# Kernel optimization log

Hardware: AMD Instinct MI355X
Metric: run time of the kernel (lower is better)

Reference implementation:

```python
import jax, jax.numpy as jnp
import numpy as np

H = 64
VOCAB = 128
LN_EPS = 1e-5
NORM_EPS = 1e-12


def _l2norm(k):
    # F.normalize(..., dim=-1): x / max(||x||_2, eps)
    n = jnp.sqrt(jnp.sum(k * k, axis=-1, keepdims=True))
    return k / jnp.maximum(n, NORM_EPS)


def _delta_scan(M0, ks, vs):
    # ks, vs: [L, B, H] time-major; M0: [B, H, H]
    def step(M, kv):
        k, v = kv
        Mk = jnp.einsum('bij,bj->bi', M, k)            # [B,H]
        M = M + (v - Mk)[:, :, None] * k[:, None, :]   # rank-1 update
        return M, None
    M, _ = jax.lax.scan(step, M0, (ks, vs))
    return M


def reference(x, embed, W1, b1, W2, b2, ln_g, ln_b, Wk, Wv, Wq, Wattn, Wout, bout):
    # Encoder: embed -> residual FF -> LayerNorm
    h = embed[x]                                        # [B,L,H]
    ff = jnp.maximum(h @ W1.T + b1, 0.0) @ W2.T + b2
    z = h + ff
    mu = jnp.mean(z, axis=-1, keepdims=True)
    var = jnp.mean((z - mu) ** 2, axis=-1, keepdims=True)
    hidden = (z - mu) / jnp.sqrt(var + LN_EPS) * ln_g + ln_b  # [B,L,H]

    B, L, _ = hidden.shape
    # First delta-rule memory write over all L steps
    ks = _l2norm(hidden @ Wk.T)                         # [B,L,H]
    vs = hidden @ Wv.T                                  # [B,L,H]
    M0 = jnp.zeros((B, H, H), dtype=hidden.dtype)
    M = _delta_scan(M0, jnp.swapaxes(ks, 0, 1), jnp.swapaxes(vs, 0, 1))

    half = L // 2
    slots = jnp.swapaxes(M, 1, 2)                       # [B,H,H] = M^T
    q = hidden[:, :half, :] @ Wattn.T                   # [B,half,H]
    # bmm(q, slots^T) = q @ M
    attn = jax.nn.softmax(jnp.einsum('bth,bhk->btk', q, M) / jnp.sqrt(jnp.asarray(H, hidden.dtype)), axis=-1)
    ctx = jnp.einsum('btk,bkh->bth', attn, slots)       # [B,half,H]

    # Second delta-rule write seeded from M
    ks2 = _l2norm(ctx @ Wk.T)
    vs2 = ctx @ Wv.T
    M2 = _delta_scan(M, jnp.swapaxes(ks2, 0, 1), jnp.swapaxes(vs2, 0, 1))

    q_last = hidden[:, -1, :] @ Wq.T                    # [B,H]
    read = jnp.einsum('bij,bj->bi', M2, q_last)         # [B,H]
    return read @ Wout.T + bout                         # [B,VOCAB]


def setup_inputs() -> dict:
    key = jax.random.key(0)
    ks = jax.random.split(key, 16)
    B, L = 64, 4096
    s = 0.05
    return {
        'x': jax.random.randint(ks[0], (B, L), 0, VOCAB),
        'embed': jax.random.normal(ks[1], (VOCAB, H), jnp.float32) * s,
        'W1': jax.random.normal(ks[2], (2 * H, H), jnp.float32) * s,
        'b1': jnp.zeros((2 * H,), jnp.float32),
        'W2': jax.random.normal(ks[3], (H, 2 * H), jnp.float32) * s,
        'b2': jnp.zeros((H,), jnp.float32),
        'ln_g': jnp.ones((H,), jnp.float32),
        'ln_b': jnp.zeros((H,), jnp.float32),
        'Wk': jax.random.normal(ks[4], (H, H), jnp.float32) * s,
        'Wv': jax.random.normal(ks[5], (H, H), jnp.float32) * s,
        'Wq': jax.random.normal(ks[6], (H, H), jnp.float32) * s,
        'Wattn': jax.random.normal(ks[7], (H, H), jnp.float32) * s,
        'Wout': jax.random.normal(ks[8], (VOCAB, H), jnp.float32) * s,
        'bout': jnp.zeros((VOCAB,), jnp.float32),
    }
```

## Files before the change

kernel.cpp:

```cpp
#include <hip/hip_runtime.h>

#define SEQL 4096
#define NB 64

__device__ __forceinline__ float dpp_xor1_add(float x) {
    int v = __builtin_amdgcn_mov_dpp(__float_as_int(x), 0xB1, 0xF, 0xF, true);
    return x + __int_as_float(v);
}
__device__ __forceinline__ float dpp_xor2_add(float x) {
    int v = __builtin_amdgcn_mov_dpp(__float_as_int(x), 0x4E, 0xF, 0xF, true);
    return x + __int_as_float(v);
}

#define FMA16(A, W, H)                                      \
    A[0]  = fmaf(W.x, H.x, A[0]);  A[1]  = fmaf(W.x, H.y, A[1]);   \
    A[2]  = fmaf(W.x, H.z, A[2]);  A[3]  = fmaf(W.x, H.w, A[3]);   \
    A[4]  = fmaf(W.y, H.x, A[4]);  A[5]  = fmaf(W.y, H.y, A[5]);   \
    A[6]  = fmaf(W.y, H.z, A[6]);  A[7]  = fmaf(W.y, H.w, A[7]);   \
    A[8]  = fmaf(W.z, H.x, A[8]);  A[9]  = fmaf(W.z, H.y, A[9]);   \
    A[10] = fmaf(W.z, H.z, A[10]); A[11] = fmaf(W.z, H.w, A[11]);  \
    A[12] = fmaf(W.w, H.x, A[12]); A[13] = fmaf(W.w, H.y, A[13]);  \
    A[14] = fmaf(W.w, H.z, A[14]); A[15] = fmaf(W.w, H.w, A[15])

__device__ __forceinline__ void proj_tile64(const float* __restrict__ sW,
                                            const float* __restrict__ sA,
                                            int jq, int tq, float* __restrict__ a)
{
#pragma unroll
    for (int u = 0; u < 16; ++u) a[u] = 0.f;
#pragma unroll 2
    for (int i = 0; i < 64; ++i) {
        float4 w  = *reinterpret_cast<const float4*>(&sW[i * 68 + jq]);
        float4 h4 = *reinterpret_cast<const float4*>(&sA[i * 68 + tq]);
        FMA16(a, w, h4);
    }
}

__device__ __forceinline__ void stage_w_t(const float* __restrict__ W, int ldw, int col0,
                                          float* __restrict__ sWb, int tid)
{
#pragma unroll
    for (int it = 0; it < 4; ++it) {
        int item = it * 256 + tid;
        int j = item & 63, cq = item >> 6;
        float4 w = *reinterpret_cast<const float4*>(&W[(size_t)j * ldw + col0 + cq * 4]);
        sWb[(cq * 4 + 0) * 68 + j] = w.x;
        sWb[(cq * 4 + 1) * 68 + j] = w.y;
        sWb[(cq * 4 + 2) * 68 + j] = w.z;
        sWb[(cq * 4 + 3) * 68 + j] = w.w;
    }
}

__device__ __forceinline__ void stage_w_n(const float* __restrict__ W,
                                          float* __restrict__ sWb, int tid)
{
#pragma unroll
    for (int it = 0; it < 4; ++it) {
        int item = it * 256 + tid;
        int r = item >> 4, c4 = item & 15;
        float4 w = *reinterpret_cast<const float4*>(&W[(size_t)r * 64 + c4 * 4]);
        *reinterpret_cast<float4*>(&sWb[r * 68 + c4 * 4]) = w;
    }
}

__global__ __launch_bounds__(256) void encoder_kernel(
    const int* __restrict__ x, const float* __restrict__ embed,
    const float* __restrict__ W1, const float* __restrict__ b1,
    const float* __restrict__ W2, const float* __restrict__ b2,
    const float* __restrict__ ln_g, const float* __restrict__ ln_b,
    const float* __restrict__ Wk, const float* __restrict__ Wv,
    const float* __restrict__ Wq, const float* __restrict__ Wattn,
    float* __restrict__ ks, float* __restrict__ vs,
    float* __restrict__ qbuf, float* __restrict__ qlast)
{
    __shared__ __align__(16) float sZ[64 * 68];
    __shared__ __align__(16) float sF[64 * 68];
    __shared__ __align__(16) float sW[64 * 68];

    const int tid = threadIdx.x;
    const size_t g0 = (size_t)blockIdx.x * 64;
    const int b = (int)(g0 >> 12);
    const int l0 = (int)(g0 & (SEQL - 1));
    const int jq = (tid & 15) * 4;
    const int tq = (tid >> 4) * 4;

    for (int idx = tid; idx < 4096; idx += 256) {
        int t = idx >> 6, i = idx & 63;
        sZ[i * 68 + t] = embed[(size_t)x[g0 + t] * 64 + i];
    }

    float zacc[16];
#pragma unroll
    for (int u = 0; u < 16; ++u) zacc[u] = 0.f;
    for (int ph = 0; ph < 2; ++ph) {
        if (ph) __syncthreads();
        stage_w_t(W1 + (size_t)ph * 64 * 64, 64, 0, sW, tid);
        __syncthreads();
        float a[16];
        proj_tile64(sW, sZ, jq, tq, a);
        float4 bb = *reinterpret_cast<const float4*>(&b1[ph * 64 + jq]);
        float bv[4] = {bb.x, bb.y, bb.z, bb.w};
#pragma unroll
        for (int u = 0; u < 4; ++u) {
            float4 o;
            o.x = fmaxf(a[u * 4 + 0] + bv[u], 0.f);
            o.y = fmaxf(a[u * 4 + 1] + bv[u], 0.f);
            o.z = fmaxf(a[u * 4 + 2] + bv[u], 0.f);
            o.w = fmaxf(a[u * 4 + 3] + bv[u], 0.f);
            *reinterpret_cast<float4*>(&sF[(jq + u) * 68 + tq]) = o;
        }
        __syncthreads();
        stage_w_t(W2, 128, ph * 64, sW, tid);
        __syncthreads();
#pragma unroll 2
        for (int p = 0; p < 64; ++p) {
            float4 w  = *reinterpret_cast<const float4*>(&sW[p * 68 + jq]);
            float4 f4 = *reinterpret_cast<const float4*>(&sF[p * 68 + tq]);
            FMA16(zacc, w, f4);
        }
    }

    {
        float z[16];
        float4 b2v = *reinterpret_cast<const float4*>(&b2[jq]);
        float bv[4] = {b2v.x, b2v.y, b2v.z, b2v.w};
#pragma unroll
        for (int u = 0; u < 4; ++u) {
            float4 h4 = *reinterpret_cast<const float4*>(&sZ[(jq + u) * 68 + tq]);
            z[u * 4 + 0] = h4.x + bv[u] + zacc[u * 4 + 0];
            z[u * 4 + 1] = h4.y + bv[u] + zacc[u * 4 + 1];
            z[u * 4 + 2] = h4.z + bv[u] + zacc[u * 4 + 2];
            z[u * 4 + 3] = h4.w + bv[u] + zacc[u * 4 + 3];
        }
        float s[4], ss[4];
#pragma unroll
        for (int v = 0; v < 4; ++v) {
            s[v]  = z[v] + z[4 + v] + z[8 + v] + z[12 + v];
            ss[v] = z[v] * z[v] + z[4 + v] * z[4 + v]
                  + z[8 + v] * z[8 + v] + z[12 + v] * z[12 + v];
        }
#pragma unroll
        for (int m = 1; m <= 8; m <<= 1) {
#pragma unroll
            for (int v = 0; v < 4; ++v) {
                s[v]  += __shfl_xor(s[v], m);
                ss[v] += __shfl_xor(ss[v], m);
            }
        }
        float mu[4], inv[4];
#pragma unroll
        for (int v = 0; v < 4; ++v) {
            mu[v] = s[v] * 0.015625f;
            float var = ss[v] * 0.015625f - mu[v] * mu[v];
            inv[v] = rsqrtf(var + 1e-5f);
        }
        float4 g4  = *reinterpret_cast<const float4*>(&ln_g[jq]);
        float4 be4 = *reinterpret_cast<const float4*>(&ln_b[jq]);
        float gv[4] = {g4.x, g4.y, g4.z, g4.w};
        float bev[4] = {be4.x, be4.y, be4.z, be4.w};
#pragma unroll
        for (int u = 0; u < 4; ++u) {
            float4 o;
            o.x = (z[u * 4 + 0] - mu[0]) * inv[0] * gv[u] + bev[u];
            o.y = (z[u * 4 + 1] - mu[1]) * inv[1] * gv[u] + bev[u];
            o.z = (z[u * 4 + 2] - mu[2]) * inv[2] * gv[u] + bev[u];
            o.w = (z[u * 4 + 3] - mu[3]) * inv[3] * gv[u] + bev[u];
            *reinterpret_cast<float4*>(&sZ[(jq + u) * 68 + tq]) = o;
        }
    }

    {
        __syncthreads();
        stage_w_t(Wk, 64, 0, sW, tid);
        __syncthreads();
        float a[16];
        proj_tile64(sW, sZ, jq, tq, a);
        float ssq[4];
#pragma unroll
        for (int v = 0; v < 4; ++v)
            ssq[v] = a[v] * a[v] + a[4 + v] * a[4 + v]
                   + a[8 + v] * a[8 + v] + a[12 + v] * a[12 + v];
#pragma unroll
        for (int m = 1; m <= 8; m <<= 1) {
#pragma unroll
            for (int v = 0; v < 4; ++v) ssq[v] += __shfl_xor(ssq[v], m);
        }
#pragma unroll
        for (int v = 0; v < 4; ++v) {
            float sc = 1.f / fmaxf(sqrtf(ssq[v]), 1e-12f);
            float4 o = make_float4(a[v] * sc, a[4 + v] * sc, a[8 + v] * sc, a[12 + v] * sc);
            *reinterpret_cast<float4*>(&ks[(g0 + tq + v) * 64 + jq]) = o;
        }
    }

    {
        __syncthreads();
        stage_w_t(Wv, 64, 0, sW, tid);
        __syncthreads();
        float a[16];
        proj_tile64(sW, sZ, jq, tq, a);
#pragma unroll
        for (int v = 0; v < 4; ++v) {
            float4 o = make_float4(a[v], a[4 + v], a[8 + v], a[12 + v]);
            *reinterpret_cast<float4*>(&vs[(g0 + tq + v) * 64 + jq]) = o;
        }
    }

    if (l0 < 2048) {
        __syncthreads();
        stage_w_t(Wattn, 64, 0, sW, tid);
        __syncthreads();
        float a[16];
        proj_tile64(sW, sZ, jq, tq, a);
#pragma unroll
        for (int v = 0; v < 4; ++v) {
            float4 o = make_float4(a[v], a[4 + v], a[8 + v], a[12 + v]);
            *reinterpret_cast<float4*>(&qbuf[((size_t)b * 2048 + l0 + tq + v) * 64 + jq]) = o;
        }
    }

    if (l0 == SEQL - 64) {
        __syncthreads();
        stage_w_t(Wq, 64, 0, sW, tid);
        __syncthreads();
        float a[16];
        proj_tile64(sW, sZ, jq, tq, a);
        if ((tid >> 4) == 15) {
            float4 o = make_float4(a[3], a[7], a[11], a[15]);
            *reinterpret_cast<float4*>(&qlast[(size_t)b * 64 + jq]) = o;
        }
    }
}

#define STEP2(K0, K1, K2, K3, V)                                                \
    do {                                                                        \
        float dp0 = fmaf(p[0], K0.x, fmaf(p[1], K0.y, fmaf(p[2], K0.z, p[3] * K0.w))); \
        float dp1 = fmaf(p[4], K1.x, fmaf(p[5], K1.y, fmaf(p[6], K1.z, p[7] * K1.w))); \
        float dp2 = fmaf(p[8], K2.x, fmaf(p[9], K2.y, fmaf(p[10], K2.z, p[11] * K2.w))); \
        float dp3 = fmaf(p[12], K3.x, fmaf(p[13], K3.y, fmaf(p[14], K3.z, p[15] * K3.w))); \
        float dq0 = fmaf(q[0], K0.x, fmaf(q[1], K0.y, fmaf(q[2], K0.z, q[3] * K0.w))); \
        float dq1 = fmaf(q[4], K1.x, fmaf(q[5], K1.y, fmaf(q[6], K1.z, q[7] * K1.w))); \
        float dq2 = fmaf(q[8], K2.x, fmaf(q[9], K2.y, fmaf(q[10], K2.z, q[11] * K2.w))); \
        float dq3 = fmaf(q[12], K3.x, fmaf(q[13], K3.y, fmaf(q[14], K3.z, q[15] * K3.w))); \
        float ddp = (dp0 + dp1) + (dp2 + dp3);                                  \
        float ddq = (dq0 + dq1) + (dq2 + dq3);                                  \
        ddp = dpp_xor1_add(ddp);  ddq = dpp_xor1_add(ddq);                      \
        ddp = dpp_xor2_add(ddp);  ddq = dpp_xor2_add(ddq);                      \
        float up = -ddp;                                                        \
        float uq = V - ddq;                                                     \
        p[0] = fmaf(up, K0.x, p[0]);   q[0] = fmaf(uq, K0.x, q[0]);             \
        p[1] = fmaf(up, K0.y, p[1]);   q[1] = fmaf(uq, K0.y, q[1]);             \
        p[2] = fmaf(up, K0.z, p[2]);   q[2] = fmaf(uq, K0.z, q[2]);             \
        p[3] = fmaf(up, K0.w, p[3]);   q[3] = fmaf(uq, K0.w, q[3]);             \
        p[4] = fmaf(up, K1.x, p[4]);   q[4] = fmaf(uq, K1.x, q[4]);             \
        p[5] = fmaf(up, K1.y, p[5]);   q[5] = fmaf(uq, K1.y, q[5]);             \
        p[6] = fmaf(up, K1.z, p[6]);   q[6] = fmaf(uq, K1.z, q[6]);             \
        p[7] = fmaf(up, K1.w, p[7]);   q[7] = fmaf(uq, K1.w, q[7]);             \
        p[8] = fmaf(up, K2.x, p[8]);   q[8] = fmaf(uq, K2.x, q[8]);             \
        p[9] = fmaf(up, K2.y, p[9]);   q[9] = fmaf(uq, K2.y, q[9]);             \
        p[10] = fmaf(up, K2.z, p[10]); q[10] = fmaf(uq, K2.z, q[10]);           \
        p[11] = fmaf(up, K2.w, p[11]); q[11] = fmaf(uq, K2.w, q[11]);           \
        p[12] = fmaf(up, K3.x, p[12]); q[12] = fmaf(uq, K3.x, q[12]);           \
        p[13] = fmaf(up, K3.y, p[13]); q[13] = fmaf(uq, K3.y, q[13]);           \
        p[14] = fmaf(up, K3.z, p[14]); q[14] = fmaf(uq, K3.z, q[14]);           \
        p[15] = fmaf(up, K3.w, p[15]); q[15] = fmaf(uq, K3.w, q[15]);           \
    } while (0)

__global__ __launch_bounds__(256) void chunk_kernel(
    float* __restrict__ ksb, float* __restrict__ vsb, int C)
{
    __shared__ __align__(16) float sk[2][32 * 64];
    __shared__ __align__(16) float sv[2][32 * 64];

    const int job = blockIdx.x;
    const int tid = threadIdx.x;
    const int r = tid >> 2;
    const int c0 = (tid & 3) * 16;
    float* kc = ksb + (size_t)job * C * 64;
    float* vc = vsb + (size_t)job * C * 64;

    float p[16], q[16];
#pragma unroll
    for (int j = 0; j < 16; ++j) { p[j] = (c0 + j == r) ? 1.f : 0.f; q[j] = 0.f; }

    const int nt = C >> 5;
    float4 rk0, rk1, rv0, rv1;

    {
        const float4* gk = reinterpret_cast<const float4*>(kc);
        const float4* gv = reinterpret_cast<const float4*>(vc);
        float4 a0 = gk[tid], a1 = gk[256 + tid];
        float4 b0 = gv[tid], b1 = gv[256 + tid];
        float4* dk = reinterpret_cast<float4*>(sk[0]);
        float4* dv = reinterpret_cast<float4*>(sv[0]);
        dk[tid] = a0; dk[256 + tid] = a1;
        dv[tid] = b0; dv[256 + tid] = b1;
    }
    if (nt > 1) {
        const float4* gk = reinterpret_cast<const float4*>(kc + 2048);
        const float4* gv = reinterpret_cast<const float4*>(vc + 2048);
        rk0 = gk[tid]; rk1 = gk[256 + tid];
        rv0 = gv[tid]; rv1 = gv[256 + tid];
    }
    __syncthreads();

    int cur = 0;
    for (int tile = 0; tile < nt; ++tile) {
        if (tile + 1 < nt) {
            float4* dk = reinterpret_cast<float4*>(sk[cur ^ 1]);
            float4* dv = reinterpret_cast<float4*>(sv[cur ^ 1]);
            dk[tid] = rk0; dk[256 + tid] = rk1;
            dv[tid] = rv0; dv[256 + tid] = rv1;
            if (tile + 2 < nt) {
                const float4* gk = reinterpret_cast<const float4*>(kc + (size_t)(tile + 2) * 2048);
                const float4* gv = reinterpret_cast<const float4*>(vc + (size_t)(tile + 2) * 2048);
                rk0 = gk[tid]; rk1 = gk[256 + tid];
                rv0 = gv[tid]; rv1 = gv[256 + tid];
            }
        }

        const float* kl = sk[cur] + c0;
        const float* vl = sv[cur] + r;
        float4 a0, a1, a2, a3, e0, e1, e2, e3;
        float va, ve;
        {
            const float4* kp = reinterpret_cast<const float4*>(kl);
            a0 = kp[0]; a1 = kp[1]; a2 = kp[2]; a3 = kp[3];
            va = vl[0];
        }
#pragma unroll
        for (int t = 0; t < 32; t += 2) {
            {
                const float4* kp = reinterpret_cast<const float4*>(kl + (t + 1) * 64);
                e0 = kp[0]; e1 = kp[1]; e2 = kp[2]; e3 = kp[3];
                ve = vl[(t + 1) * 64];
            }
            STEP2(a0, a1, a2, a3, va);
            if (t + 2 < 32) {
                const float4* kp = reinterpret_cast<const float4*>(kl + (t + 2) * 64);
                a0 = kp[0]; a1 = kp[1]; a2 = kp[2]; a3 = kp[3];
                va = vl[(t + 2) * 64];
            }
            STEP2(e0, e1, e2, e3, ve);
        }
        __syncthreads();
        cur ^= 1;
    }

    float4* po = reinterpret_cast<float4*>(kc + r * 64 + c0);
    po[0] = make_float4(p[0], p[1], p[2], p[3]);
    po[1] = make_float4(p[4], p[5], p[6], p[7]);
    po[2] = make_float4(p[8], p[9], p[10], p[11]);
    po[3] = make_float4(p[12], p[13], p[14], p[15]);
    float4* qo = reinterpret_cast<float4*>(vc + r * 64 + c0);
    qo[0] = make_float4(q[0], q[1], q[2], q[3]);
    qo[1] = make_float4(q[4], q[5], q[6], q[7]);
    qo[2] = make_float4(q[8], q[9], q[10], q[11]);
    qo[3] = make_float4(q[12], q[13], q[14], q[15]);
}

__global__ __launch_bounds__(256) void combine_kernel(
    const float* __restrict__ Pb, const float* __restrict__ Qb,
    const float* __restrict__ Min, float* __restrict__ Mout,
    int nc, int chunk_stride)
{
    __shared__ __align__(16) float sM[2][64 * 68];
    __shared__ __align__(16) float sP[2][64 * 64];
    const int b = blockIdx.x;
    const int tid = threadIdx.x;
    const int r = tid >> 2;
    const int j0 = (tid & 3) * 16;

    if (Min) {
        const float4* mi = reinterpret_cast<const float4*>(Min + ((size_t)b * 64 + r) * 64 + j0);
        float4* mo = reinterpret_cast<float4*>(&sM[0][r * 68 + j0]);
#pragma unroll
        for (int u = 0; u < 4; ++u) mo[u] = mi[u];
    } else {
#pragma unroll
        for (int u = 0; u < 16; ++u) sM[0][r * 68 + j0 + u] = 0.f;
    }
    {
        const float4* g = reinterpret_cast<const float4*>(Pb + (size_t)b * nc * chunk_stride);
        float4* s = reinterpret_cast<float4*>(sP[0]);
        for (int i = tid; i < 1024; i += 256) s[i] = g[i];
    }
    __syncthreads();

    int cur = 0;
    for (int c = 0; c < nc; ++c) {
        const size_t cbase = (size_t)(b * nc + c) * chunk_stride;
        float4 rp0, rp1, rp2, rp3;
        if (c + 1 < nc) {
            const float4* g = reinterpret_cast<const float4*>(Pb + cbase + chunk_stride);
            rp0 = g[tid]; rp1 = g[tid + 256]; rp2 = g[tid + 512]; rp3 = g[tid + 768];
        }
        float4 rq0, rq1, rq2, rq3;
        {
            const float4* gq = reinterpret_cast<const float4*>(Qb + cbase + r * 64 + j0);
            rq0 = gq[0]; rq1 = gq[1]; rq2 = gq[2]; rq3 = gq[3];
        }
        float acc[16];
#pragma unroll
        for (int u = 0; u < 16; ++u) acc[u] = 0.f;
        const float* Mrow = &sM[cur][r * 68];
        const float* Pl = sP[c & 1];
#pragma unroll
        for (int mg = 0; mg < 16; ++mg) {
            float4 a = *reinterpret_cast<const float4*>(Mrow + mg * 4);
#pragma unroll
            for (int e2 = 0; e2 < 4; ++e2) {
                float am = (e2 == 0) ? a.x : (e2 == 1) ? a.y : (e2 == 2) ? a.z : a.w;
                const float4* pr = reinterpret_cast<const float4*>(Pl + (mg * 4 + e2) * 64 + j0);
                float4 p0 = pr[0], p1 = pr[1], p2 = pr[2], p3 = pr[3];
                acc[0] = fmaf(am, p0.x, acc[0]);  acc[1] = fmaf(am, p0.y, acc[1]);
                acc[2] = fmaf(am, p0.z, acc[2]);  acc[3] = fmaf(am, p0.w, acc[3]);
                acc[4] = fmaf(am, p1.x, acc[4]);  acc[5] = fmaf(am, p1.y, acc[5]);
                acc[6] = fmaf(am, p1.z, acc[6]);  acc[7] = fmaf(am, p1.w, acc[7]);
                acc[8] = fmaf(am, p2.x, acc[8]);  acc[9] = fmaf(am, p2.y, acc[9]);
                acc[10] = fmaf(am, p2.z, acc[10]); acc[11] = fmaf(am, p2.w, acc[11]);
                acc[12] = fmaf(am, p3.x, acc[12]); acc[13] = fmaf(am, p3.y, acc[13]);
                acc[14] = fmaf(am, p3.z, acc[14]); acc[15] = fmaf(am, p3.w, acc[15]);
            }
        }
        const int nxt = cur ^ 1;
        float* om = &sM[nxt][r * 68 + j0];
        om[0] = acc[0] + rq0.x;  om[1] = acc[1] + rq0.y;
        om[2] = acc[2] + rq0.z;  om[3] = acc[3] + rq0.w;
        om[4] = acc[4] + rq1.x;  om[5] = acc[5] + rq1.y;
        om[6] = acc[6] + rq1.z;  om[7] = acc[7] + rq1.w;
        om[8] = acc[8] + rq2.x;  om[9] = acc[9] + rq2.y;
        om[10] = acc[10] + rq2.z; om[11] = acc[11] + rq2.w;
        om[12] = acc[12] + rq3.x; om[13] = acc[13] + rq3.y;
        om[14] = acc[14] + rq3.z; om[15] = acc[15] + rq3.w;
        if (c + 1 < nc) {
            float4* s = reinterpret_cast<float4*>(sP[(c + 1) & 1]);
            s[tid] = rp0; s[tid + 256] = rp1; s[tid + 512] = rp2; s[tid + 768] = rp3;
        }
        __syncthreads();
        cur = nxt;
    }

    float4* mo = reinterpret_cast<float4*>(Mout + ((size_t)b * 64 + r) * 64 + j0);
    const float* fm = &sM[cur][r * 68 + j0];
    mo[0] = make_float4(fm[0], fm[1], fm[2], fm[3]);
    mo[1] = make_float4(fm[4], fm[5], fm[6], fm[7]);
    mo[2] = make_float4(fm[8], fm[9], fm[10], fm[11]);
    mo[3] = make_float4(fm[12], fm[13], fm[14], fm[15]);
}

__global__ __launch_bounds__(256) void attn_kernel(
    const float* __restrict__ qg, const float* __restrict__ Mbuf,
    const float* __restrict__ Wk, const float* __restrict__ Wv,
    float* __restrict__ ks2, float* __restrict__ vs2)
{
    __shared__ __align__(16) float sW1[64 * 68];
    __shared__ __align__(16) float sW2[64 * 68];
    __shared__ __align__(16) float sA[64 * 68];
    __shared__ __align__(16) float sB[64 * 68];

    const int b = blockIdx.y;
    const int tile0 = blockIdx.x * 64;
    const int tid = threadIdx.x;
    const int jq = (tid & 15) * 4;
    const int tq = (tid >> 4) * 4;
    const size_t qbase = (size_t)b * 2048 + tile0;
    const float* Mb = Mbuf + (size_t)b * 4096;

    stage_w_n(Mb, sW1, tid);
    stage_w_t(Mb, 64, 0, sW2, tid);
    stage_w_t(qg + qbase * 64, 64, 0, sA, tid);
    __syncthreads();

    float a[16];
    proj_tile64(sW1, sA, jq, tq, a);
#pragma unroll
    for (int u = 0; u < 16; ++u) a[u] *= 0.125f;

    {
        float mx[4], sm[4];
#pragma unroll
        for (int v = 0; v < 4; ++v)
            mx[v] = fmaxf(fmaxf(a[v], a[4 + v]), fmaxf(a[8 + v], a[12 + v]));
#pragma unroll
        for (int m = 1; m <= 8; m <<= 1) {
#pragma unroll
            for (int v = 0; v < 4; ++v) mx[v] = fmaxf(mx[v], __shfl_xor(mx[v], m));
        }
#pragma unroll
        for (int v = 0; v < 4; ++v) {
            a[v]      = __expf(a[v]      - mx[v]);
            a[4 + v]  = __expf(a[4 + v]  - mx[v]);
            a[8 + v]  = __expf(a[8 + v]  - mx[v]);
            a[12 + v] = __expf(a[12 + v] - mx[v]);
            sm[v] = a[v] + a[4 + v] + a[8 + v] + a[12 + v];
        }
#pragma unroll
        for (int m = 1; m <= 8; m <<= 1) {
#pragma unroll
            for (int v = 0; v < 4; ++v) sm[v] += __shfl_xor(sm[v], m);
        }
        float rinv[4];
#pragma unroll
        for (int v = 0; v < 4; ++v) rinv[v] = 1.f / sm[v];
#pragma unroll
        for (int v = 0; v < 4; ++v) {
            a[v] *= rinv[v]; a[4 + v] *= rinv[v];
            a[8 + v] *= rinv[v]; a[12 + v] *= rinv[v];
        }
    }
#pragma unroll
    for (int u = 0; u < 4; ++u)
        *reinterpret_cast<float4*>(&sB[(jq + u) * 68 + tq]) =
            make_float4(a[u * 4 + 0], a[u * 4 + 1], a[u * 4 + 2], a[u * 4 + 3]);
    __syncthreads();

    float c[16];
    proj_tile64(sW2, sB, jq, tq, c);
#pragma unroll
    for (int u = 0; u < 4; ++u)
        *reinterpret_cast<float4*>(&sA[(jq + u) * 68 + tq]) =
            make_float4(c[u * 4 + 0], c[u * 4 + 1], c[u * 4 + 2], c[u * 4 + 3]);
    __syncthreads();

    stage_w_t(Wk, 64, 0, sW1, tid);
    stage_w_t(Wv, 64, 0, sW2, tid);
    __syncthreads();

    float ak[16], av[16];
#pragma unroll
    for (int u = 0; u < 16; ++u) { ak[u] = 0.f; av[u] = 0.f; }
#pragma unroll 2
    for (int i = 0; i < 64; ++i) {
        float4 wk = *reinterpret_cast<const float4*>(&sW1[i * 68 + jq]);
        float4 wv = *reinterpret_cast<const float4*>(&sW2[i * 68 + jq]);
        float4 c4 = *reinterpret_cast<const float4*>(&sA[i * 68 + tq]);
        FMA16(ak, wk, c4);
        FMA16(av, wv, c4);
    }

    {
        float ssq[4];
#pragma unroll
        for (int v = 0; v < 4; ++v)
            ssq[v] = ak[v] * ak[v] + ak[4 + v] * ak[4 + v]
                   + ak[8 + v] * ak[8 + v] + ak[12 + v] * ak[12 + v];
#pragma unroll
        for (int m = 1; m <= 8; m <<= 1) {
#pragma unroll
            for (int v = 0; v < 4; ++v) ssq[v] += __shfl_xor(ssq[v], m);
        }
#pragma unroll
        for (int v = 0; v < 4; ++v) {
            float sc = 1.f / fmaxf(sqrtf(ssq[v]), 1e-12f);
            const size_t o = (qbase + tq + v) * 64 + jq;
            *reinterpret_cast<float4*>(&ks2[o]) =
                make_float4(ak[v] * sc, ak[4 + v] * sc, ak[8 + v] * sc, ak[12 + v] * sc);
            *reinterpret_cast<float4*>(&vs2[o]) =
                make_float4(av[v], av[4 + v], av[8 + v], av[12 + v]);
        }
    }
}

__global__ __launch_bounds__(128) void out_kernel(
    const float* __restrict__ M2, const float* __restrict__ qlast,
    const float* __restrict__ Wout, const float* __restrict__ bout,
    float* __restrict__ out)
{
    const int b = blockIdx.x;
    const int tid = threadIdx.x;
    __shared__ float sq[64], sread[64];
    if (tid < 64) sq[tid] = qlast[b * 64 + tid];
    __syncthreads();
    if (tid < 64) {
        const float* Mr = M2 + ((size_t)b * 64 + tid) * 64;
        float acc = 0.f;
        for (int j = 0; j < 64; ++j) acc = fmaf(Mr[j], sq[j], acc);
        sread[tid] = acc;
    }
    __syncthreads();
    float acc = bout[tid];
    for (int h = 0; h < 64; ++h) acc = fmaf(Wout[tid * 64 + h], sread[h], acc);
    out[b * 128 + tid] = acc;
}

extern "C" void kernel_launch(void* const* d_in, const int* in_sizes, int n_in,
                              void* d_out, int out_size, void* d_ws, size_t ws_size,
                              hipStream_t stream)
{
    const int* x        = (const int*)d_in[0];
    const float* embed  = (const float*)d_in[1];
    const float* W1     = (const float*)d_in[2];
    const float* b1     = (const float*)d_in[3];
    const float* W2     = (const float*)d_in[4];
    const float* b2     = (const float*)d_in[5];
    const float* ln_g   = (const float*)d_in[6];
    const float* ln_b   = (const float*)d_in[7];
    const float* Wk     = (const float*)d_in[8];
    const float* Wv     = (const float*)d_in[9];
    const float* Wq     = (const float*)d_in[10];
    const float* Wattn  = (const float*)d_in[11];
    const float* Wout   = (const float*)d_in[12];
    const float* bout   = (const float*)d_in[13];

    float* ws = (float*)d_ws;
    float* ks = ws;
    float* vs = ks + (size_t)NB * SEQL * 64;
    float* qb = vs + (size_t)NB * SEQL * 64;
    float* ql = qb + (size_t)NB * 2048 * 64;
    float* M  = ql + (size_t)NB * 64;
    float* M2 = M + (size_t)NB * 64 * 64;
    if (ws_size < (size_t)(M2 + (size_t)NB * 64 * 64 - ws) * sizeof(float)) return;

    hipLaunchKernelGGL(encoder_kernel, dim3((NB * SEQL) / 64), dim3(256), 0, stream,
                       x, embed, W1, b1, W2, b2, ln_g, ln_b, Wk, Wv, Wq, Wattn,
                       ks, vs, qb, ql);

    const int C1 = 256, nc1 = SEQL / C1;
    hipLaunchKernelGGL(chunk_kernel, dim3(NB * nc1), dim3(256), 0, stream, ks, vs, C1);
    hipLaunchKernelGGL(combine_kernel, dim3(NB), dim3(256), 0, stream,
                       ks, vs, (const float*)nullptr, M, nc1, C1 * 64);

    hipLaunchKernelGGL(attn_kernel, dim3(32, NB), dim3(256), 0, stream,
                       qb, M, Wk, Wv, ks, vs);

    const int C2 = 128, nc2 = 2048 / C2;
    hipLaunchKernelGGL(chunk_kernel, dim3(NB * nc2), dim3(256), 0, stream, ks, vs, C2);
    hipLaunchKernelGGL(combine_kernel, dim3(NB), dim3(256), 0, stream,
                       ks, vs, M, M2, nc2, C2 * 64);

    hipLaunchKernelGGL(out_kernel, dim3(NB), dim3(128), 0, stream,
                       M2, ql, Wout, bout, (float*)d_out);
}
```

Before: 567.3 us.

## Prefetch encoder weights into registers and split combine across row blocks

The encoder kernel now loads each upcoming weight matrix into registers while the current projection runs, and stages Wk and Wv at the same time into separate shared buffers. This removes serial global-load-then-sync stalls, at the cost of extra registers. The combine kernel is split four ways by row block, so each block updates only 16 rows of M. That raises the grid from 64 to 256 blocks, but each block still loads the full P chunk into shared memory. Projection loop unroll factors are also raised from 2 to 4.

```diff
diff --git a/kernel.cpp b/kernel.cpp
--- a/kernel.cpp
+++ b/kernel.cpp
@@ -28,7 +28,7 @@
 {
 #pragma unroll
     for (int u = 0; u < 16; ++u) a[u] = 0.f;
-#pragma unroll 2
+#pragma unroll 4
     for (int i = 0; i < 64; ++i) {
         float4 w  = *reinterpret_cast<const float4*>(&sW[i * 68 + jq]);
         float4 h4 = *reinterpret_cast<const float4*>(&sA[i * 68 + tq]);
@@ -36,21 +36,37 @@
     }
 }
 
+__device__ __forceinline__ void load_w_t(const float* __restrict__ W, int ldw, int col0,
+                                         int tid, float4* __restrict__ r)
+{
+    const int j = tid & 63;
+    const int cq0 = tid >> 6;
+#pragma unroll
+    for (int it = 0; it < 4; ++it)
+        r[it] = *reinterpret_cast<const float4*>(&W[(size_t)j * ldw + col0 + (it * 4 + cq0) * 4]);
+}
+__device__ __forceinline__ void write_w_t(const float4* __restrict__ r,
+                                          float* __restrict__ sWb, int tid)
+{
+    const int j = tid & 63;
+    const int cq0 = tid >> 6;
+#pragma unroll
+    for (int it = 0; it < 4; ++it) {
+        const int c = (it * 4 + cq0) * 4;
+        sWb[(c + 0) * 68 + j] = r[it].x;
+        sWb[(c + 1) * 68 + j] = r[it].y;
+        sWb[(c + 2) * 68 + j] = r[it].z;
+        sWb[(c + 3) * 68 + j] = r[it].w;
+    }
+}
+
 __device__ __forceinline__ void stage_w_t(const float* __restrict__ W, int ldw, int col0,
                                           float* __restrict__ sWb, int tid)
 {
-#pragma unroll
-    for (int it = 0; it < 4; ++it) {
-        int item = it * 256 + tid;
-        int j = item & 63, cq = item >> 6;
-        float4 w = *reinterpret_cast<const float4*>(&W[(size_t)j * ldw + col0 + cq * 4]);
-        sWb[(cq * 4 + 0) * 68 + j] = w.x;
-        sWb[(cq * 4 + 1) * 68 + j] = w.y;
-        sWb[(cq * 4 + 2) * 68 + j] = w.z;
-        sWb[(cq * 4 + 3) * 68 + j] = w.w;
-    }
-}
-
+    float4 r[4];
+    load_w_t(W, ldw, col0, tid, r);
+    write_w_t(r, sWb, tid);
+}
 __device__ __forceinline__ void stage_w_n(const float* __restrict__ W,
                                           float* __restrict__ sWb, int tid)
 {
@@ -83,22 +99,28 @@
     const int l0 = (int)(g0 & (SEQL - 1));
     const int jq = (tid & 15) * 4;
     const int tq = (tid >> 4) * 4;
-
+    const bool doq = (l0 < 2048);
+    const bool dolast = (l0 == SEQL - 64);
+
+    float4 pf[4], pf2[4];
+
+    load_w_t(W1, 64, 0, tid, pf);
     for (int idx = tid; idx < 4096; idx += 256) {
         int t = idx >> 6, i = idx & 63;
         sZ[i * 68 + t] = embed[(size_t)x[g0 + t] * 64 + i];
     }
+    write_w_t(pf, sW, tid);
+    load_w_t(W2, 128, 0, tid, pf2);
+    __syncthreads();
 
     float zacc[16];
 #pragma unroll
     for (int u = 0; u < 16; ++u) zacc[u] = 0.f;
-    for (int ph = 0; ph < 2; ++ph) {
-        if (ph) __syncthreads();
-        stage_w_t(W1 + (size_t)ph * 64 * 64, 64, 0, sW, tid);
-        __syncthreads();
+
+    {
         float a[16];
         proj_tile64(sW, sZ, jq, tq, a);
-        float4 bb = *reinterpret_cast<const float4*>(&b1[ph * 64 + jq]);
+        float4 bb = *reinterpret_cast<const float4*>(&b1[jq]);
         float bv[4] = {bb.x, bb.y, bb.z, bb.w};
 #pragma unroll
         for (int u = 0; u < 4; ++u) {
@@ -109,15 +131,46 @@
             o.w = fmaxf(a[u * 4 + 3] + bv[u], 0.f);
             *reinterpret_cast<float4*>(&sF[(jq + u) * 68 + tq]) = o;
         }
-        __syncthreads();
-        stage_w_t(W2, 128, ph * 64, sW, tid);
-        __syncthreads();
-#pragma unroll 2
-        for (int p = 0; p < 64; ++p) {
-            float4 w  = *reinterpret_cast<const float4*>(&sW[p * 68 + jq]);
-            float4 f4 = *reinterpret_cast<const float4*>(&sF[p * 68 + tq]);
-            FMA16(zacc, w, f4);
-        }
+    }
+    __syncthreads();
+    write_w_t(pf2, sW, tid);
+    load_w_t(W1 + 4096, 64, 0, tid, pf);
+    __syncthreads();
+#pragma unroll 4
+    for (int p = 0; p < 64; ++p) {
+        float4 w  = *reinterpret_cast<const float4*>(&sW[p * 68 + jq]);
+        float4 f4 = *reinterpret_cast<const float4*>(&sF[p * 68 + tq]);
+        FMA16(zacc, w, f4);
+    }
+    __syncthreads();
+    write_w_t(pf, sW, tid);
+    load_w_t(W2, 128, 64, tid, pf2);
+    __syncthreads();
+    {
+        float a[16];
+        proj_tile64(sW, sZ, jq, tq, a);
+        float4 bb = *reinterpret_cast<const float4*>(&b1[64 + jq]);
+        float bv[4] = {bb.x, bb.y, bb.z, bb.w};
+#pragma unroll
+        for (int u = 0; u < 4; ++u) {
+            float4 o;
+            o.x = fmaxf(a[u * 4 + 0] + bv[u], 0.f);
+            o.y = fmaxf(a[u * 4 + 1] + bv[u], 0.f);
+            o.z = fmaxf(a[u * 4 + 2] + bv[u], 0.f);
+            o.w = fmaxf(a[u * 4 + 3] + bv[u], 0.f);
+            *reinterpret_cast<float4*>(&sF[(jq + u) * 68 + tq]) = o;
+        }
+    }
+    __syncthreads();
+    write_w_t(pf2, sW, tid);
+    load_w_t(Wk, 64, 0, tid, pf);
+    load_w_t(Wv, 64, 0, tid, pf2);
+    __syncthreads();
+#pragma unroll 4
+    for (int p = 0; p < 64; ++p) {
+        float4 w  = *reinterpret_cast<const float4*>(&sW[p * 68 + jq]);
+        float4 f4 = *reinterpret_cast<const float4*>(&sF[p * 68 + tq]);
+        FMA16(zacc, w, f4);
     }
 
     {
@@ -168,11 +221,14 @@
             *reinterpret_cast<float4*>(&sZ[(jq + u) * 68 + tq]) = o;
         }
     }
-
-    {
-        __syncthreads();
-        stage_w_t(Wk, 64, 0, sW, tid);
-        __syncthreads();
+    __syncthreads();
+    write_w_t(pf, sW, tid);
+    write_w_t(pf2, sF, tid);
+    if (doq)        load_w_t(Wattn, 64, 0, tid, pf);
+    else if (dolast) load_w_t(Wq, 64, 0, tid, pf);
+    __syncthreads();
+
+    {
         float a[16];
         proj_tile64(sW, sZ, jq, tq, a);
         float ssq[4];
@@ -192,40 +248,29 @@
             *reinterpret_cast<float4*>(&ks[(g0 + tq + v) * 64 + jq]) = o;
         }
     }
-
-    {
+    {
+        float a[16];
+        proj_tile64(sF, sZ, jq, tq, a);
+#pragma unroll
+        for (int v = 0; v < 4; ++v) {
+            float4 o = make_float4(a[v], a[4 + v], a[8 + v], a[12 + v]);
+            *reinterpret_cast<float4*>(&vs[(g0 + tq + v) * 64 + jq]) = o;
+        }
+    }
+
+    if (doq || dolast) {
         __syncthreads();
-        stage_w_t(Wv, 64, 0, sW, tid);
+        write_w_t(pf, sW, tid);
         __syncthreads();
         float a[16];
         proj_tile64(sW, sZ, jq, tq, a);
-#pragma unroll
-        for (int v = 0; v < 4; ++v) {
-            float4 o = make_float4(a[v], a[4 + v], a[8 + v], a[12 + v]);
-            *reinterpret_cast<float4*>(&vs[(g0 + tq + v) * 64 + jq]) = o;
-        }
-    }
-
-    if (l0 < 2048) {
-        __syncthreads();
-        stage_w_t(Wattn, 64, 0, sW, tid);
-        __syncthreads();
-        float a[16];
-        proj_tile64(sW, sZ, jq, tq, a);
-#pragma unroll
-        for (int v = 0; v < 4; ++v) {
-            float4 o = make_float4(a[v], a[4 + v], a[8 + v], a[12 + v]);
-            *reinterpret_cast<float4*>(&qbuf[((size_t)b * 2048 + l0 + tq + v) * 64 + jq]) = o;
-        }
-    }
-
-    if (l0 == SEQL - 64) {
-        __syncthreads();
-        stage_w_t(Wq, 64, 0, sW, tid);
-        __syncthreads();
-        float a[16];
-        proj_tile64(sW, sZ, jq, tq, a);
-        if ((tid >> 4) == 15) {
+        if (doq) {
+#pragma unroll
+            for (int v = 0; v < 4; ++v) {
+                float4 o = make_float4(a[v], a[4 + v], a[8 + v], a[12 + v]);
+                *reinterpret_cast<float4*>(&qbuf[((size_t)b * 2048 + l0 + tq + v) * 64 + jq]) = o;
+            }
+        } else if ((tid >> 4) == 15) {
             float4 o = make_float4(a[3], a[7], a[11], a[15]);
             *reinterpret_cast<float4*>(&qlast[(size_t)b * 64 + jq]) = o;
         }
@@ -364,21 +409,21 @@
     const float* __restrict__ Min, float* __restrict__ Mout,
     int nc, int chunk_stride)
 {
-    __shared__ __align__(16) float sM[2][64 * 68];
     __shared__ __align__(16) float sP[2][64 * 64];
-    const int b = blockIdx.x;
+    __shared__ __align__(16) float sM[2][16 * 68];
+    const int bb = blockIdx.x;
+    const int b = bb >> 2;
+    const int r0 = (bb & 3) << 4;
     const int tid = threadIdx.x;
-    const int r = tid >> 2;
-    const int j0 = (tid & 3) * 16;
+    const int rl = tid >> 4;
+    const int j4 = (tid & 15) * 4;
+    const int gr = r0 + rl;
 
     if (Min) {
-        const float4* mi = reinterpret_cast<const float4*>(Min + ((size_t)b * 64 + r) * 64 + j0);
-        float4* mo = reinterpret_cast<float4*>(&sM[0][r * 68 + j0]);
-#pragma unroll
-        for (int u = 0; u < 4; ++u) mo[u] = mi[u];
+        *reinterpret_cast<float4*>(&sM[0][rl * 68 + j4]) =
+            *reinterpret_cast<const float4*>(Min + ((size_t)b * 64 + gr) * 64 + j4);
     } else {
-#pragma unroll
-        for (int u = 0; u < 16; ++u) sM[0][r * 68 + j0 + u] = 0.f;
+        *reinterpret_cast<float4*>(&sM[0][rl * 68 + j4]) = make_float4(0.f, 0.f, 0.f, 0.f);
     }
     {
         const float4* g = reinterpret_cast<const float4*>(Pb + (size_t)b * nc * chunk_stride);
@@ -395,44 +440,30 @@
             const float4* g = reinterpret_cast<const float4*>(Pb + cbase + chunk_stride);
             rp0 = g[tid]; rp1 = g[tid + 256]; rp2 = g[tid + 512]; rp3 = g[tid + 768];
         }
-        float4 rq0, rq1, rq2, rq3;
-        {
-            const float4* gq = reinterpret_cast<const float4*>(Qb + cbase + r * 64 + j0);
-            rq0 = gq[0]; rq1 = gq[1]; rq2 = gq[2]; rq3 = gq[3];
-        }
-        float acc[16];
-#pragma unroll
-        for (int u = 0; u < 16; ++u) acc[u] = 0.f;
-        const float* Mrow = &sM[cur][r * 68];
+        float4 rq = *reinterpret_cast<const float4*>(Qb + cbase + (size_t)gr * 64 + j4);
+
+        float ax = 0.f, ay = 0.f, az = 0.f, aw = 0.f;
+        const float* Mrow = &sM[cur][rl * 68];
         const float* Pl = sP[c & 1];
-#pragma unroll
+#pragma unroll 4
         for (int mg = 0; mg < 16; ++mg) {
-            float4 a = *reinterpret_cast<const float4*>(Mrow + mg * 4);
-#pragma unroll
-            for (int e2 = 0; e2 < 4; ++e2) {
-                float am = (e2 == 0) ? a.x : (e2 == 1) ? a.y : (e2 == 2) ? a.z : a.w;
-                const float4* pr = reinterpret_cast<const float4*>(Pl + (mg * 4 + e2) * 64 + j0);
-                float4 p0 = pr[0], p1 = pr[1], p2 = pr[2], p3 = pr[3];
-                acc[0] = fmaf(am, p0.x, acc[0]);  acc[1] = fmaf(am, p0.y, acc[1]);
-                acc[2] = fmaf(am, p0.z, acc[2]);  acc[3] = fmaf(am, p0.w, acc[3]);
-                acc[4] = fmaf(am, p1.x, acc[4]);  acc[5] = fmaf(am, p1.y, acc[5]);
-                acc[6] = fmaf(am, p1.z, acc[6]);  acc[7] = fmaf(am, p1.w, acc[7]);
-                acc[8] = fmaf(am, p2.x, acc[8]);  acc[9] = fmaf(am, p2.y, acc[9]);
-                acc[10] = fmaf(am, p2.z, acc[10]); acc[11] = fmaf(am, p2.w, acc[11]);
-                acc[12] = fmaf(am, p3.x, acc[12]); acc[13] = fmaf(am, p3.y, acc[13]);
-                acc[14] = fmaf(am, p3.z, acc[14]); acc[15] = fmaf(am, p3.w, acc[15]);
-            }
+            float4 a4 = *reinterpret_cast<const float4*>(Mrow + mg * 4);
+            float4 p0 = *reinterpret_cast<const float4*>(Pl + (mg * 4 + 0) * 64 + j4);
+            float4 p1 = *reinterpret_cast<const float4*>(Pl + (mg * 4 + 1) * 64 + j4);
+            float4 p2 = *reinterpret_cast<const float4*>(Pl + (mg * 4 + 2) * 64 + j4);
+            float4 p3 = *reinterpret_cast<const float4*>(Pl + (mg * 4 + 3) * 64 + j4);
+            ax = fmaf(a4.x, p0.x, ax); ay = fmaf(a4.x, p0.y, ay);
+            az = fmaf(a4.x, p0.z, az); aw = fmaf(a4.x, p0.w, aw);
+            ax = fmaf(a4.y, p1.x, ax); ay = fmaf(a4.y, p1.y, ay);
+            az = fmaf(a4.y, p1.z, az); aw = fmaf(a4.y, p1.w, aw);
+            ax = fmaf(a4.z, p2.x, ax); ay = fmaf(a4.z, p2.y, ay);
+            az = fmaf(a4.z, p2.z, az); aw = fmaf(a4.z, p2.w, aw);
+            ax = fmaf(a4.w, p3.x, ax); ay = fmaf(a4.w, p3.y, ay);
+            az = fmaf(a4.w, p3.z, az); aw = fmaf(a4.w, p3.w, aw);
         }
         const int nxt = cur ^ 1;
-        float* om = &sM[nxt][r * 68 + j0];
-        om[0] = acc[0] + rq0.x;  om[1] = acc[1] + rq0.y;
-        om[2] = acc[2] + rq0.z;  om[3] = acc[3] + rq0.w;
-        om[4] = acc[4] + rq1.x;  om[5] = acc[5] + rq1.y;
-        om[6] = acc[6] + rq1.z;  om[7] = acc[7] + rq1.w;
-        om[8] = acc[8] + rq2.x;  om[9] = acc[9] + rq2.y;
-        om[10] = acc[10] + rq2.z; om[11] = acc[11] + rq2.w;
-        om[12] = acc[12] + rq3.x; om[13] = acc[13] + rq3.y;
-        om[14] = acc[14] + rq3.z; om[15] = acc[15] + rq3.w;
+        *reinterpret_cast<float4*>(&sM[nxt][rl * 68 + j4]) =
+            make_float4(ax + rq.x, ay + rq.y, az + rq.z, aw + rq.w);
         if (c + 1 < nc) {
             float4* s = reinterpret_cast<float4*>(sP[(c + 1) & 1]);
             s[tid] = rp0; s[tid + 256] = rp1; s[tid + 512] = rp2; s[tid + 768] = rp3;
@@ -440,13 +471,8 @@
         __syncthreads();
         cur = nxt;
     }
-
-    float4* mo = reinterpret_cast<float4*>(Mout + ((size_t)b * 64 + r) * 64 + j0);
-    const float* fm = &sM[cur][r * 68 + j0];
-    mo[0] = make_float4(fm[0], fm[1], fm[2], fm[3]);
-    mo[1] = make_float4(fm[4], fm[5], fm[6], fm[7]);
-    mo[2] = make_float4(fm[8], fm[9], fm[10], fm[11]);
-    mo[3] = make_float4(fm[12], fm[13], fm[14], fm[15]);
+    *reinterpret_cast<float4*>(Mout + ((size_t)b * 64 + gr) * 64 + j4) =
+        *reinterpret_cast<const float4*>(&sM[cur][rl * 68 + j4]);
 }
 
 __global__ __launch_bounds__(256) void attn_kernel(
@@ -618,7 +644,7 @@
 
     const int C1 = 256, nc1 = SEQL / C1;
     hipLaunchKernelGGL(chunk_kernel, dim3(NB * nc1), dim3(256), 0, stream, ks, vs, C1);
-    hipLaunchKernelGGL(combine_kernel, dim3(NB), dim3(256), 0, stream,
+    hipLaunchKernelGGL(combine_kernel, dim3(NB * 4), dim3(256), 0, stream,
                        ks, vs, (const float*)nullptr, M, nc1, C1 * 64);
 
     hipLaunchKernelGGL(attn_kernel, dim3(32, NB), dim3(256), 0, stream,
@@ -626,7 +652,7 @@
 
     const int C2 = 128, nc2 = 2048 / C2;
     hipLaunchKernelGGL(chunk_kernel, dim3(NB * nc2), dim3(256), 0, stream, ks, vs, C2);
-    hipLaunchKernelGGL(combine_kernel, dim3(NB), dim3(256), 0, stream,
+    hipLaunchKernelGGL(combine_kernel, dim3(NB * 4), dim3(256), 0, stream,
                        ks, vs, M, M2, nc2, C2 * 64);
 
     hipLaunchKernelGGL(out_kernel, dim3(NB), dim3(128), 0, stream,
```

Measured after the change: 494.6 us. 12.8% less time.
